# Performance work log

Measured on AMD Instinct MI355X. Metric: run time of the kernel, lower is better.

The kernel has to match this reference:

```python
import jax, jax.numpy as jnp
import numpy as np

N_NODES = 100000
N_EDGES = 1600000


def setup_inputs() -> dict:
    key = jax.random.key(0)
    k1, k2, k3, k4, k5 = jax.random.split(key, 5)
    node_states = jax.random.normal(k1, (N_NODES, 128), dtype=jnp.float32)
    edge_index = jax.random.randint(k2, (2, N_EDGES), 0, N_NODES, dtype=jnp.int64)
    mask = jax.random.uniform(k3, (N_EDGES,), dtype=jnp.float32)  # edge weights
    # Glorot-ish init for the two GCN linear layers
    W1 = jax.random.normal(k4, (128, 64), dtype=jnp.float32) * 0.05
    b1 = jnp.zeros((64,), dtype=jnp.float32)
    W2 = jax.random.normal(k5, (64, 64), dtype=jnp.float32) * 0.05
    b2 = jnp.zeros((64,), dtype=jnp.float32)
    return {"node_states": node_states, "edge_index": edge_index, "mask": mask,
            "W1": W1, "b1": b1, "W2": W2, "b2": b2}


def _gcn_layer(x, src, dst, edge_w, W, b, n_nodes):
    # PyG GCNConv (normalize=False): h = x @ W; out[dst] += edge_w * h[src]; out += b
    h = x @ W                                  # [N, d_out]
    msg = h[src] * edge_w[:, None]             # [E, d_out] gather + scale
    agg = jax.ops.segment_sum(msg, dst, num_segments=n_nodes)  # scatter-add
    return agg + b


def reference(node_states, edge_index, mask, W1, b1, W2, b2):
    src = edge_index[0]
    dst = edge_index[1]
    n = node_states.shape[0]
    h1 = jax.nn.relu(_gcn_layer(node_states, src, dst, mask, W1, b1, n))
    h2 = jax.nn.relu(_gcn_layer(h1, src, dst, mask, W2, b2, n))
    return h2
```

## Files before the change

### kernel.cpp

```cpp
#include <hip/hip_runtime.h>
#include <hip/hip_bf16.h>

#define N_NODES 100000
#define N_EDGES 1600000
#define NB_C 391
#define NB_F 3125
#define NBLK_S 391
#define CHUNK_E 4096
#define CAPC 4608
#define QCAP 768
#define GCSTRIDE 32
#define FIXSCALE 1048576.0f
#define FIXINV   (1.0f / 1048576.0f)


typedef short v8s __attribute__((ext_vector_type(8)));
typedef float v4f __attribute__((ext_vector_type(4)));

static __device__ __forceinline__ unsigned pack_bf2(float a, float b) {
    __hip_bfloat162 p = __float22bfloat162_rn(make_float2(a, b));
    return *reinterpret_cast<unsigned*>(&p);
}
static __device__ __forceinline__ float2 bf2_to_f2(unsigned u) {
    __hip_bfloat162 p = *reinterpret_cast<__hip_bfloat162*>(&u);
    return __bfloat1622float2(p);
}

__global__ __launch_bounds__(1024) void k1_sort_gemm(const int* __restrict__ src,
                                                     const int* __restrict__ dst,
                                                     const float* __restrict__ wgt,
                                                     const float* __restrict__ x,
                                                     const float* __restrict__ W1,
                                                     int* __restrict__ gcount,
                                                     int2* __restrict__ arena,
                                                     unsigned* __restrict__ hpre) {
    __shared__ __align__(16) int smem[13976];
    const int b = blockIdx.x;
    const int t = threadIdx.x;

    if (b >= NBLK_S) {
        unsigned* xs = (unsigned*)smem;
        unsigned* ws = (unsigned*)smem + 64 * 68;
        const int tile = b - NBLK_S;
        const int row0 = tile * 64;
        {
            const float2* g2 = (const float2*)W1;
            for (int i = t; i < 64 * 128 / 2; i += 1024) {
                const float2 v = g2[i];
                const int k = (2 * i) >> 6;
                const int c = (2 * i) & 63;
                ((short*)&ws[c * 68])[k]       = (short)(pack_bf2(v.x, 0.f) & 0xFFFF);
                ((short*)&ws[(c + 1) * 68])[k] = (short)(pack_bf2(v.y, 0.f) & 0xFFFF);
            }
        }
        {
            const float4* g = (const float4*)x;
            for (int i = t; i < 64 * 32; i += 1024) {
                const int r = i >> 5, cu = i & 31;
                const int row = row0 + r;
                uint2 v = make_uint2(0u, 0u);
                if (row < N_NODES) {
                    float4 f = g[(size_t)row * 32 + cu];
                    v.x = pack_bf2(f.x, f.y);
                    v.y = pack_bf2(f.z, f.w);
                }
                *(uint2*)&xs[r * 68 + 2 * cu] = v;
            }
        }
        __syncthreads();
        const int w = t >> 6, lane = t & 63;
        const int l15 = lane & 15, quad = lane >> 4;
        const int a  = w & 3;
        const int g_ = w >> 2;
        v4f acc = (v4f){0.f, 0.f, 0.f, 0.f};
#pragma unroll
        for (int k0 = 0; k0 < 128; k0 += 32) {
            const int ku = k0 / 2 + quad * 4;
            const v8s xb = *(const v8s*)&xs[(g_ * 16 + l15) * 68 + ku];
            const v8s wa = *(const v8s*)&ws[(16 * a + l15) * 68 + ku];
            acc = __builtin_amdgcn_mfma_f32_16x16x32_bf16(wa, xb, acc, 0, 0, 0);
        }
        __syncthreads();
        float* stg = (float*)smem;
        *(v4f*)&stg[(g_ * 16 + l15) * 68 + 16 * a + 4 * quad] = acc;
        __syncthreads();
        for (int i2 = t; i2 < 2048; i2 += 1024) {
            const int nl = i2 >> 5, d = i2 & 31;
            const int row = row0 + nl;
            if (row < N_NODES)
                hpre[(size_t)row * 32 + d] = pack_bf2(stg[nl * 68 + d], stg[nl * 68 + d + 32]);
        }
        return;
    }

    int*  hist  = smem;
    int*  lcur  = smem + 391;
    int*  tgb   = smem + 782;
    int*  pairs = smem + 1173;
    int*  tg    = smem + 1685;
    int2* ord   = (int2*)(smem + 5782);

    for (int i = t; i < NB_C; i += 1024) hist[i] = 0;
    __syncthreads();

    const int e0 = b * CHUNK_E;
    const int n = min(CHUNK_E, N_EDGES - e0);
    const int nI4 = n >> 2;
    const bool act = t < nI4;
    int4 sv, dv; float4 wv;
    if (act) {
        sv = ((const int4*)(src + e0))[t];
        dv = ((const int4*)(dst + e0))[t];
        wv = ((const float4*)(wgt + e0))[t];
        atomicAdd(&hist[dv.x >> 8], 1);
        atomicAdd(&hist[dv.y >> 8], 1);
        atomicAdd(&hist[dv.z >> 8], 1);
        atomicAdd(&hist[dv.w >> 8], 1);
    }
    __syncthreads();
    if (t < 512) pairs[t] = (t < NB_C) ? hist[t] : 0;
    __syncthreads();
    for (int off = 1; off < 512; off <<= 1) {
        int u = 0;
        if (t < 512 && t >= off) u = pairs[t - off];
        __syncthreads();
        if (t < 512) pairs[t] += u;
        __syncthreads();
    }
    if (t < NB_C) lcur[t] = pairs[t] - hist[t];
    __syncthreads();
    for (int i = t; i < NB_C; i += 1024) {
        const int hv = hist[i];
        const int lb = lcur[i];
        const int grsv = (hv > 0) ? atomicAdd(&gcount[i * GCSTRIDE], hv) : 0;
        tgb[i] = i * CAPC + grsv - lb;
    }
    __syncthreads();
    if (act) {
        {
            const int bk = dv.x >> 8;
            const int lp = atomicAdd(&lcur[bk], 1);
            ord[lp] = make_int2(sv.x | ((dv.x & 255) << 17), __float_as_int(wv.x));
            tg[lp] = tgb[bk] + lp;
        }
        {
            const int bk = dv.y >> 8;
            const int lp = atomicAdd(&lcur[bk], 1);
            ord[lp] = make_int2(sv.y | ((dv.y & 255) << 17), __float_as_int(wv.y));
            tg[lp] = tgb[bk] + lp;
        }
        {
            const int bk = dv.z >> 8;
            const int lp = atomicAdd(&lcur[bk], 1);
            ord[lp] = make_int2(sv.z | ((dv.z & 255) << 17), __float_as_int(wv.z));
            tg[lp] = tgb[bk] + lp;
        }
        {
            const int bk = dv.w >> 8;
            const int lp = atomicAdd(&lcur[bk], 1);
            ord[lp] = make_int2(sv.w | ((dv.w & 255) << 17), __float_as_int(wv.w));
            tg[lp] = tgb[bk] + lp;
        }
    }
    __syncthreads();
    for (int i = t; i < n; i += 1024)
        arena[tg[i]] = ord[i];
}

template<bool FUSE>
__global__ __launch_bounds__(256) void gather_fuse(const unsigned* __restrict__ hsrc,
                                                   const int2* __restrict__ arena,
                                                   const int* __restrict__ gcount,
                                                   const float* __restrict__ bias,
                                                   const float* __restrict__ W2,
                                                   void* __restrict__ outp) {
    __shared__ int accs[32 * 68];
    __shared__ int2 qrec[QCAP];
    __shared__ int qn_s;
    extern __shared__ unsigned wsdyn[];
    const int t = threadIdx.x;

    const int orig = blockIdx.x;
    const int xcd = orig & 7, idx = orig >> 3;
    const int b = (xcd < 5 ? xcd * 391 : 5 * 391 + (xcd - 5) * 390) + idx;

    const int cb = b >> 3;
    const int sub = b & 7;
    for (int i = t; i < 2048; i += 256) accs[i] = 0;
    if (t == 0) qn_s = 0;
    if constexpr (FUSE) {
        const float2* g2 = (const float2*)W2;
        for (int i = t; i < 2048; i += 256) {
            const float2 v = g2[i];
            const int k = (2 * i) >> 6;
            const int c = (2 * i) & 63;
            ((short*)&wsdyn[c * 36])[k]       = (short)(pack_bf2(v.x, 0.f) & 0xFFFF);
            ((short*)&wsdyn[(c + 1) * 36])[k] = (short)(pack_bf2(v.y, 0.f) & 0xFFFF);
        }
    }
    __syncthreads();

    const int lane = t & 63;
    {
        const int cntc = min(gcount[cb * GCSTRIDE], CAPC);
        const size_t cbase = (size_t)cb * CAPC;
        const unsigned long long below = (lane == 63) ? ~0ull >> 1
                                                      : (1ull << lane) - 1;
        for (int i = t; i < cntc; i += 256) {
            const int2 r = arena[cbase + i];
            const bool keep = ((r.x >> 22) & 7) == sub;
            const unsigned long long m = __ballot(keep);
            int base = 0;
            if (lane == 0) base = atomicAdd(&qn_s, __popcll(m));
            base = __builtin_amdgcn_readfirstlane(base);
            if (keep) {
                const int pos = base + __popcll(m & below);
                if (pos < QCAP) qrec[pos] = r;
            }
        }
    }
    __syncthreads();
    const int qn = min(qn_s, QCAP);
    const int npad = (qn + 63) & ~63;
    for (int i = qn + t; i < npad; i += 256) qrec[i] = make_int2(0, 0);
    __syncthreads();

    const int li2 = t & 15;
    const int s   = t >> 4;
    const int qw  = s & 3;
    const int m   = (li2 + 4 * qw) & 15;
    const int p   = qw & 1;
    for (int ib = s; ib < npad; ib += 64) {
        int2 r[4];
#pragma unroll
        for (int j = 0; j < 4; ++j) r[j] = qrec[ib + 16 * j];
        uint2 hv[4];
#pragma unroll
        for (int j = 0; j < 4; ++j)
            hv[j] = *(const uint2*)&hsrc[(size_t)(r[j].x & 0x1FFFF) * 32 + 2 * m];
#pragma unroll
        for (int j = 0; j < 4; ++j) {
            const int dl = (r[j].x >> 17) & 31;
            const float wsf = __int_as_float(r[j].y) * FIXSCALE;
            const float2 fa = bf2_to_f2(hv[j].x);
            const float2 fb = bf2_to_f2(hv[j].y);
            int* ap = &accs[dl * 64 + 2 * m];
            const float v0 = p ? fb.x : fa.x;
            const float v1 = p ? fa.x : fb.x;
            const float v2 = p ? fb.y : fa.y;
            const float v3 = p ? fa.y : fb.y;
            atomicAdd(ap + p,          (int)(wsf * v0));
            atomicAdd(ap + 1 - p,      (int)(wsf * v1));
            atomicAdd(ap + 32 + p,     (int)(wsf * v2));
            atomicAdd(ap + 33 - p,     (int)(wsf * v3));
        }
    }
    __syncthreads();

    if constexpr (FUSE) {
        unsigned pk[4];
#pragma unroll
        for (int k = 0; k < 4; ++k) {
            const int i2 = t + k * 256;
            const int node = i2 >> 5, cp = i2 & 31;
            const float f0 = fmaxf((float)accs[node * 64 + 2 * cp]     * FIXINV + bias[2 * cp],     0.f);
            const float f1 = fmaxf((float)accs[node * 64 + 2 * cp + 1] * FIXINV + bias[2 * cp + 1], 0.f);
            pk[k] = pack_bf2(f0, f1);
        }
        __syncthreads();
        unsigned* xs = (unsigned*)accs;
#pragma unroll
        for (int k = 0; k < 4; ++k) {
            const int i2 = t + k * 256;
            xs[(i2 >> 5) * 36 + (i2 & 31)] = pk[k];
        }
        __syncthreads();
        const int l15 = lane & 15, quad = lane >> 4;
        const int w = t >> 6;
        v4f a0 = (v4f){0.f, 0.f, 0.f, 0.f};
        v4f a1 = (v4f){0.f, 0.f, 0.f, 0.f};
#pragma unroll
        for (int k0 = 0; k0 < 64; k0 += 32) {
            const int ku = k0 / 2 + quad * 4;
            const v8s wa  = *(const v8s*)&wsdyn[(16 * w + l15) * 36 + ku];
            const v8s xb0 = *(const v8s*)&xs[l15 * 36 + ku];
            const v8s xb1 = *(const v8s*)&xs[(16 + l15) * 36 + ku];
            a0 = __builtin_amdgcn_mfma_f32_16x16x32_bf16(wa, xb0, a0, 0, 0, 0);
            a1 = __builtin_amdgcn_mfma_f32_16x16x32_bf16(wa, xb1, a1, 0, 0, 0);
        }
        __syncthreads();
        float* stg = (float*)accs;
        *(v4f*)&stg[l15 * 68 + 16 * w + 4 * quad] = a0;
        *(v4f*)&stg[(16 + l15) * 68 + 16 * w + 4 * quad] = a1;
        __syncthreads();
        for (int i2 = t; i2 < 1024; i2 += 256) {
            const int nl = i2 >> 5, d = i2 & 31;
            const int ng = b * 32 + nl;
            ((unsigned*)outp)[(size_t)ng * 32 + d] =
                pack_bf2(stg[nl * 68 + d], stg[nl * 68 + d + 32]);
        }
    } else {
        for (int i2 = t; i2 < 1024; i2 += 256) {
            const int node = i2 >> 5, cp = i2 & 31;
            const int ng = b * 32 + node;
            float2 o;
            o.x = fmaxf((float)accs[node * 64 + 2 * cp]     * FIXINV + bias[2 * cp],     0.f);
            o.y = fmaxf((float)accs[node * 64 + 2 * cp + 1] * FIXINV + bias[2 * cp + 1], 0.f);
            *(float2*)&((float*)outp)[(size_t)ng * 64 + 2 * cp] = o;
        }
    }
}

extern "C" void kernel_launch(void* const* d_in, const int* in_sizes, int n_in,
                              void* d_out, int out_size, void* d_ws, size_t ws_size,
                              hipStream_t stream) {
    const float* x    = (const float*)d_in[0];
    const int*   eidx = (const int*)d_in[1];
    const float* mask = (const float*)d_in[2];
    const float* W1   = (const float*)d_in[3];
    const float* b1   = (const float*)d_in[4];
    const float* W2   = (const float*)d_in[5];
    const float* b2   = (const float*)d_in[6];
    float* out = (float*)d_out;

    const int* src = eidx;
    const int* dst = eidx + N_EDGES;

    unsigned* hpre = (unsigned*)d_out;

    int2*     arena  = (int2*)d_ws;
    int*      gcount = (int*)(arena + (size_t)NB_C * CAPC);
    unsigned* hpre2  = (unsigned*)(gcount + NB_C * GCSTRIDE);

    const int gemmBlocks = (N_NODES + 63) / 64;

    hipMemsetAsync(gcount, 0, NB_C * GCSTRIDE * sizeof(int), stream);

    k1_sort_gemm<<<NBLK_S + gemmBlocks, 1024, 0, stream>>>(src, dst, mask, x, W1,
                                                           gcount, arena, hpre);

    gather_fuse<true><<<NB_F, 256, 64 * 36 * 4, stream>>>(hpre, arena, gcount,
                                                          b1, W2, hpre2);
    gather_fuse<false><<<NB_F, 256, 0, stream>>>(hpre2, arena, gcount,
                                                 b2, nullptr, out);
}
```

Baseline: 227.1 us.

## Bucket edges by 128-node groups and have gather blocks read buckets directly

The sort stage now bins edges into 782 buckets of 128 destination nodes, where it used 391 buckets of 256. Each gather block owns one whole bucket and reads it straight from the arena. This removes the old step where 8 sub-blocks each scanned a 256-node bucket and filtered it through a ballot/atomic queue in shared memory. Blocks grow to 512 threads with a 128-node accumulator, the fused second-layer GEMM is redone as two 64-node passes that write results directly, and the XCD block remapping is dropped. The risks are fewer, larger blocks (lower occupancy and parallelism), per-bucket capacity truncation at CAPB, and a longer 1024-wide scan in the sort kernel.

```diff
diff --git a/kernel.cpp b/kernel.cpp
--- a/kernel.cpp
+++ b/kernel.cpp
@@ -3,12 +3,10 @@
 
 #define N_NODES 100000
 #define N_EDGES 1600000
-#define NB_C 391
-#define NB_F 3125
+#define NB_B 782
 #define NBLK_S 391
 #define CHUNK_E 4096
-#define CAPC 4608
-#define QCAP 768
+#define CAPB 2432
 #define GCSTRIDE 32
 #define FIXSCALE 1048576.0f
 #define FIXINV   (1.0f / 1048576.0f)
@@ -34,7 +32,7 @@
                                                      int* __restrict__ gcount,
                                                      int2* __restrict__ arena,
                                                      unsigned* __restrict__ hpre) {
-    __shared__ __align__(16) int smem[13976];
+    __shared__ __align__(16) int smem[15660];
     const int b = blockIdx.x;
     const int t = threadIdx.x;
 
@@ -94,13 +92,13 @@
     }
 
     int*  hist  = smem;
-    int*  lcur  = smem + 391;
-    int*  tgb   = smem + 782;
-    int*  pairs = smem + 1173;
-    int*  tg    = smem + 1685;
-    int2* ord   = (int2*)(smem + 5782);
-
-    for (int i = t; i < NB_C; i += 1024) hist[i] = 0;
+    int*  lcur  = smem + 782;
+    int*  tgb   = smem + 1564;
+    int*  pairs = smem + 2346;
+    int*  tg    = smem + 3370;
+    int2* ord   = (int2*)(smem + 7466);
+
+    for (int i = t; i < NB_B; i += 1024) hist[i] = 0;
     __syncthreads();
 
     const int e0 = b * CHUNK_E;
@@ -112,53 +110,52 @@
         sv = ((const int4*)(src + e0))[t];
         dv = ((const int4*)(dst + e0))[t];
         wv = ((const float4*)(wgt + e0))[t];
-        atomicAdd(&hist[dv.x >> 8], 1);
-        atomicAdd(&hist[dv.y >> 8], 1);
-        atomicAdd(&hist[dv.z >> 8], 1);
-        atomicAdd(&hist[dv.w >> 8], 1);
-    }
-    __syncthreads();
-    if (t < 512) pairs[t] = (t < NB_C) ? hist[t] : 0;
-    __syncthreads();
-    for (int off = 1; off < 512; off <<= 1) {
-        int u = 0;
-        if (t < 512 && t >= off) u = pairs[t - off];
-        __syncthreads();
-        if (t < 512) pairs[t] += u;
-        __syncthreads();
-    }
-    if (t < NB_C) lcur[t] = pairs[t] - hist[t];
-    __syncthreads();
-    for (int i = t; i < NB_C; i += 1024) {
+        atomicAdd(&hist[dv.x >> 7], 1);
+        atomicAdd(&hist[dv.y >> 7], 1);
+        atomicAdd(&hist[dv.z >> 7], 1);
+        atomicAdd(&hist[dv.w >> 7], 1);
+    }
+    __syncthreads();
+    pairs[t] = (t < NB_B) ? hist[t] : 0;
+    __syncthreads();
+    for (int off = 1; off < 1024; off <<= 1) {
+        const int u = (t >= off) ? pairs[t - off] : 0;
+        __syncthreads();
+        pairs[t] += u;
+        __syncthreads();
+    }
+    if (t < NB_B) lcur[t] = pairs[t] - hist[t];
+    __syncthreads();
+    for (int i = t; i < NB_B; i += 1024) {
         const int hv = hist[i];
         const int lb = lcur[i];
         const int grsv = (hv > 0) ? atomicAdd(&gcount[i * GCSTRIDE], hv) : 0;
-        tgb[i] = i * CAPC + grsv - lb;
+        tgb[i] = i * CAPB + grsv - lb;
     }
     __syncthreads();
     if (act) {
         {
-            const int bk = dv.x >> 8;
+            const int bk = dv.x >> 7;
             const int lp = atomicAdd(&lcur[bk], 1);
-            ord[lp] = make_int2(sv.x | ((dv.x & 255) << 17), __float_as_int(wv.x));
+            ord[lp] = make_int2(sv.x | ((dv.x & 127) << 17), __float_as_int(wv.x));
             tg[lp] = tgb[bk] + lp;
         }
         {
-            const int bk = dv.y >> 8;
+            const int bk = dv.y >> 7;
             const int lp = atomicAdd(&lcur[bk], 1);
-            ord[lp] = make_int2(sv.y | ((dv.y & 255) << 17), __float_as_int(wv.y));
+            ord[lp] = make_int2(sv.y | ((dv.y & 127) << 17), __float_as_int(wv.y));
             tg[lp] = tgb[bk] + lp;
         }
         {
-            const int bk = dv.z >> 8;
+            const int bk = dv.z >> 7;
             const int lp = atomicAdd(&lcur[bk], 1);
-            ord[lp] = make_int2(sv.z | ((dv.z & 255) << 17), __float_as_int(wv.z));
+            ord[lp] = make_int2(sv.z | ((dv.z & 127) << 17), __float_as_int(wv.z));
             tg[lp] = tgb[bk] + lp;
         }
         {
-            const int bk = dv.w >> 8;
+            const int bk = dv.w >> 7;
             const int lp = atomicAdd(&lcur[bk], 1);
-            ord[lp] = make_int2(sv.w | ((dv.w & 255) << 17), __float_as_int(wv.w));
+            ord[lp] = make_int2(sv.w | ((dv.w & 127) << 17), __float_as_int(wv.w));
             tg[lp] = tgb[bk] + lp;
         }
     }
@@ -168,29 +165,21 @@
 }
 
 template<bool FUSE>
-__global__ __launch_bounds__(256) void gather_fuse(const unsigned* __restrict__ hsrc,
+__global__ __launch_bounds__(512) void gather_fuse(const unsigned* __restrict__ hsrc,
                                                    const int2* __restrict__ arena,
                                                    const int* __restrict__ gcount,
                                                    const float* __restrict__ bias,
                                                    const float* __restrict__ W2,
                                                    void* __restrict__ outp) {
-    __shared__ int accs[32 * 68];
-    __shared__ int2 qrec[QCAP];
-    __shared__ int qn_s;
+    __shared__ int accs[128 * 64];
     extern __shared__ unsigned wsdyn[];
     const int t = threadIdx.x;
-
-    const int orig = blockIdx.x;
-    const int xcd = orig & 7, idx = orig >> 3;
-    const int b = (xcd < 5 ? xcd * 391 : 5 * 391 + (xcd - 5) * 390) + idx;
-
-    const int cb = b >> 3;
-    const int sub = b & 7;
-    for (int i = t; i < 2048; i += 256) accs[i] = 0;
-    if (t == 0) qn_s = 0;
+    const int b = blockIdx.x;
+
+    for (int i = t; i < 8192; i += 512) accs[i] = 0;
     if constexpr (FUSE) {
         const float2* g2 = (const float2*)W2;
-        for (int i = t; i < 2048; i += 256) {
+        for (int i = t; i < 2048; i += 512) {
             const float2 v = g2[i];
             const int k = (2 * i) >> 6;
             const int c = (2 * i) & 63;
@@ -200,48 +189,30 @@
     }
     __syncthreads();
 
-    const int lane = t & 63;
-    {
-        const int cntc = min(gcount[cb * GCSTRIDE], CAPC);
-        const size_t cbase = (size_t)cb * CAPC;
-        const unsigned long long below = (lane == 63) ? ~0ull >> 1
-                                                      : (1ull << lane) - 1;
-        for (int i = t; i < cntc; i += 256) {
-            const int2 r = arena[cbase + i];
-            const bool keep = ((r.x >> 22) & 7) == sub;
-            const unsigned long long m = __ballot(keep);
-            int base = 0;
-            if (lane == 0) base = atomicAdd(&qn_s, __popcll(m));
-            base = __builtin_amdgcn_readfirstlane(base);
-            if (keep) {
-                const int pos = base + __popcll(m & below);
-                if (pos < QCAP) qrec[pos] = r;
-            }
-        }
-    }
-    __syncthreads();
-    const int qn = min(qn_s, QCAP);
-    const int npad = (qn + 63) & ~63;
-    for (int i = qn + t; i < npad; i += 256) qrec[i] = make_int2(0, 0);
-    __syncthreads();
-
+    const int cnt = min(gcount[b * GCSTRIDE], CAPB);
+    const size_t base = (size_t)b * CAPB;
     const int li2 = t & 15;
     const int s   = t >> 4;
     const int qw  = s & 3;
     const int m   = (li2 + 4 * qw) & 15;
     const int p   = qw & 1;
-    for (int ib = s; ib < npad; ib += 64) {
-        int2 r[4];
-#pragma unroll
-        for (int j = 0; j < 4; ++j) r[j] = qrec[ib + 16 * j];
+    for (int ib = s; ib < cnt; ib += 128) {
+        int2 r[4]; float wf[4];
+#pragma unroll
+        for (int j = 0; j < 4; ++j) {
+            const int idx = ib + 32 * j;
+            const bool v = idx < cnt;
+            r[j] = arena[base + (v ? idx : 0)];
+            wf[j] = v ? __int_as_float(r[j].y) : 0.f;
+        }
         uint2 hv[4];
 #pragma unroll
         for (int j = 0; j < 4; ++j)
             hv[j] = *(const uint2*)&hsrc[(size_t)(r[j].x & 0x1FFFF) * 32 + 2 * m];
 #pragma unroll
         for (int j = 0; j < 4; ++j) {
-            const int dl = (r[j].x >> 17) & 31;
-            const float wsf = __int_as_float(r[j].y) * FIXSCALE;
+            const int dl = (r[j].x >> 17) & 127;
+            const float wsf = wf[j] * FIXSCALE;
             const float2 fa = bf2_to_f2(hv[j].x);
             const float2 fb = bf2_to_f2(hv[j].y);
             int* ap = &accs[dl * 64 + 2 * m];
@@ -257,56 +228,62 @@
     }
     __syncthreads();
 
+    const int lane = t & 63;
     if constexpr (FUSE) {
-        unsigned pk[4];
-#pragma unroll
-        for (int k = 0; k < 4; ++k) {
-            const int i2 = t + k * 256;
-            const int node = i2 >> 5, cp = i2 & 31;
-            const float f0 = fmaxf((float)accs[node * 64 + 2 * cp]     * FIXINV + bias[2 * cp],     0.f);
-            const float f1 = fmaxf((float)accs[node * 64 + 2 * cp + 1] * FIXINV + bias[2 * cp + 1], 0.f);
-            pk[k] = pack_bf2(f0, f1);
-        }
-        __syncthreads();
-        unsigned* xs = (unsigned*)accs;
-#pragma unroll
-        for (int k = 0; k < 4; ++k) {
-            const int i2 = t + k * 256;
-            xs[(i2 >> 5) * 36 + (i2 & 31)] = pk[k];
-        }
-        __syncthreads();
         const int l15 = lane & 15, quad = lane >> 4;
         const int w = t >> 6;
-        v4f a0 = (v4f){0.f, 0.f, 0.f, 0.f};
-        v4f a1 = (v4f){0.f, 0.f, 0.f, 0.f};
-#pragma unroll
-        for (int k0 = 0; k0 < 64; k0 += 32) {
-            const int ku = k0 / 2 + quad * 4;
-            const v8s wa  = *(const v8s*)&wsdyn[(16 * w + l15) * 36 + ku];
-            const v8s xb0 = *(const v8s*)&xs[l15 * 36 + ku];
-            const v8s xb1 = *(const v8s*)&xs[(16 + l15) * 36 + ku];
-            a0 = __builtin_amdgcn_mfma_f32_16x16x32_bf16(wa, xb0, a0, 0, 0, 0);
-            a1 = __builtin_amdgcn_mfma_f32_16x16x32_bf16(wa, xb1, a1, 0, 0, 0);
-        }
-        __syncthreads();
-        float* stg = (float*)accs;
-        *(v4f*)&stg[l15 * 68 + 16 * w + 4 * quad] = a0;
-        *(v4f*)&stg[(16 + l15) * 68 + 16 * w + 4 * quad] = a1;
-        __syncthreads();
-        for (int i2 = t; i2 < 1024; i2 += 256) {
-            const int nl = i2 >> 5, d = i2 & 31;
-            const int ng = b * 32 + nl;
-            ((unsigned*)outp)[(size_t)ng * 32 + d] =
-                pack_bf2(stg[nl * 68 + d], stg[nl * 68 + d + 32]);
+        const int g = w >> 1;
+        const int cpw = w & 1;
+        for (int q = 0; q < 2; ++q) {
+            unsigned pk[4];
+#pragma unroll
+            for (int k = 0; k < 4; ++k) {
+                const int i2 = t + k * 512;
+                const int node = i2 >> 5, cp = i2 & 31;
+                const int* ac = &accs[(q * 64 + node) * 64 + 2 * cp];
+                const float f0 = fmaxf((float)ac[0] * FIXINV + bias[2 * cp],     0.f);
+                const float f1 = fmaxf((float)ac[1] * FIXINV + bias[2 * cp + 1], 0.f);
+                pk[k] = pack_bf2(f0, f1);
+            }
+            __syncthreads();
+            unsigned* xs = (unsigned*)&accs[q * 4096];
+#pragma unroll
+            for (int k = 0; k < 4; ++k) {
+                const int i2 = t + k * 512;
+                xs[(i2 >> 5) * 36 + (i2 & 31)] = pk[k];
+            }
+            __syncthreads();
+            v4f a0 = (v4f){0.f, 0.f, 0.f, 0.f};
+            v4f a1 = (v4f){0.f, 0.f, 0.f, 0.f};
+#pragma unroll
+            for (int k0 = 0; k0 < 64; k0 += 32) {
+                const int ku = k0 / 2 + quad * 4;
+                const v8s xb  = *(const v8s*)&xs[(g * 16 + l15) * 36 + ku];
+                const v8s wa0 = *(const v8s*)&wsdyn[(16 * cpw + l15) * 36 + ku];
+                const v8s wa1 = *(const v8s*)&wsdyn[(16 * (cpw + 2) + l15) * 36 + ku];
+                a0 = __builtin_amdgcn_mfma_f32_16x16x32_bf16(wa0, xb, a0, 0, 0, 0);
+                a1 = __builtin_amdgcn_mfma_f32_16x16x32_bf16(wa1, xb, a1, 0, 0, 0);
+            }
+            const int ng = b * 128 + q * 64 + g * 16 + l15;
+            if (ng < N_NODES) {
+                uint4 o;
+                o.x = pack_bf2(a0[0], a1[0]);
+                o.y = pack_bf2(a0[1], a1[1]);
+                o.z = pack_bf2(a0[2], a1[2]);
+                o.w = pack_bf2(a0[3], a1[3]);
+                *(uint4*)&((unsigned*)outp)[(size_t)ng * 32 + 16 * cpw + 4 * quad] = o;
+            }
         }
     } else {
-        for (int i2 = t; i2 < 1024; i2 += 256) {
+        for (int i2 = t; i2 < 4096; i2 += 512) {
             const int node = i2 >> 5, cp = i2 & 31;
-            const int ng = b * 32 + node;
-            float2 o;
-            o.x = fmaxf((float)accs[node * 64 + 2 * cp]     * FIXINV + bias[2 * cp],     0.f);
-            o.y = fmaxf((float)accs[node * 64 + 2 * cp + 1] * FIXINV + bias[2 * cp + 1], 0.f);
-            *(float2*)&((float*)outp)[(size_t)ng * 64 + 2 * cp] = o;
+            const int ng = b * 128 + node;
+            if (ng < N_NODES) {
+                float2 o;
+                o.x = fmaxf((float)accs[node * 64 + 2 * cp]     * FIXINV + bias[2 * cp],     0.f);
+                o.y = fmaxf((float)accs[node * 64 + 2 * cp + 1] * FIXINV + bias[2 * cp + 1], 0.f);
+                *(float2*)&((float*)outp)[(size_t)ng * 64 + 2 * cp] = o;
+            }
         }
     }
 }
@@ -329,18 +306,18 @@
     unsigned* hpre = (unsigned*)d_out;
 
     int2*     arena  = (int2*)d_ws;
-    int*      gcount = (int*)(arena + (size_t)NB_C * CAPC);
-    unsigned* hpre2  = (unsigned*)(gcount + NB_C * GCSTRIDE);
+    int*      gcount = (int*)(arena + (size_t)NB_B * CAPB);
+    unsigned* hpre2  = (unsigned*)(gcount + NB_B * GCSTRIDE);
 
     const int gemmBlocks = (N_NODES + 63) / 64;
 
-    hipMemsetAsync(gcount, 0, NB_C * GCSTRIDE * sizeof(int), stream);
+    hipMemsetAsync(gcount, 0, NB_B * GCSTRIDE * sizeof(int), stream);
 
     k1_sort_gemm<<<NBLK_S + gemmBlocks, 1024, 0, stream>>>(src, dst, mask, x, W1,
                                                            gcount, arena, hpre);
 
-    gather_fuse<true><<<NB_F, 256, 64 * 36 * 4, stream>>>(hpre, arena, gcount,
+    gather_fuse<true><<<NB_B, 512, 64 * 36 * 4, stream>>>(hpre, arena, gcount,
                                                           b1, W2, hpre2);
-    gather_fuse<false><<<NB_F, 256, 0, stream>>>(hpre2, arena, gcount,
+    gather_fuse<false><<<NB_B, 512, 0, stream>>>(hpre2, arena, gcount,
                                                  b2, nullptr, out);
 }
```

After: 240.6 us. 1.06x slower.
